# Optimization experiments

Hardware: AMD Instinct MI355X
Metric: run time of the kernel (lower is better)

The kernel has to match this reference:

```python
import jax, jax.numpy as jnp
import numpy as np

N_EXPERTS = 8
TOP_K = 2
D_MODEL = 1024
N_TOKENS = 8192


def setup_inputs() -> dict:
    key = jax.random.key(0)
    k1, k2, k3, k4, k5 = jax.random.split(key, 5)
    x = jax.random.normal(k1, (N_TOKENS, D_MODEL), dtype=jnp.float32)
    # router Linear(num_experts): weight [d, E], bias [E]
    Wr = jax.random.normal(k2, (D_MODEL, N_EXPERTS), dtype=jnp.float32) / np.sqrt(D_MODEL)
    br = jnp.zeros((N_EXPERTS,), dtype=jnp.float32)
    # per-expert Linear(d_model): stacked weights [E, d, d], biases [E, d]
    W = jax.random.normal(k3, (N_EXPERTS, D_MODEL, D_MODEL), dtype=jnp.float32) / np.sqrt(D_MODEL)
    b = jnp.zeros((N_EXPERTS, D_MODEL), dtype=jnp.float32)
    return {"x": x, "Wr": Wr, "br": br, "W": W, "b": b}


def reference(x, Wr, br, W, b):
    # --- route ---
    logits = x @ Wr + br                                  # [N, E]
    top_k_vals, top_k_idxs = jax.lax.top_k(logits, TOP_K)  # [N, k]
    top_k_gates = jax.nn.softmax(top_k_vals, axis=-1)      # [N, k]
    # --- experts (dense form of gather-dispatch; same math as routed compute) ---
    y_all = jnp.einsum('nd,edh->neh', x, W) + b            # [N, E, d]
    # --- gather routed expert outputs per slot ---
    y_k = jnp.take_along_axis(y_all, top_k_idxs[:, :, None], axis=1)  # [N, k, d]
    # --- weighted scatter-combine (reduce) ---
    out = jnp.sum(top_k_gates[:, :, None] * y_k, axis=1)   # [N, d]
    return out
```

## Files before the change

### kernel.cpp

```cpp
#include <hip/hip_runtime.h>
#include <hip/hip_bf16.h>


#define NTOK 8192
#define DM   1024
#define NEXP 8
#define CAP  8192
#define MAXT 136

typedef __attribute__((ext_vector_type(8))) short bf16x8;
typedef __attribute__((ext_vector_type(4))) float f32x4;

__device__ __forceinline__ unsigned short f2bf(float f) {
  unsigned u = __float_as_uint(f);
  unsigned r = (u + 0x7fffu + ((u >> 16) & 1u)) >> 16;
  return (unsigned short)r;
}
__device__ __forceinline__ float bf2f(unsigned short s) {
  return __uint_as_float(((unsigned)s) << 16);
}

__device__ __forceinline__ void gl_lds16(const void* g, void* l) {
  __builtin_amdgcn_global_load_lds(
      (const __attribute__((address_space(1))) unsigned int*)g,
      (__attribute__((address_space(3))) unsigned int*)l, 16, 0, 0);
}

__global__ __launch_bounds__(256) void transpose_w_kernel(
    const float* __restrict__ W, unsigned short* __restrict__ Wt) {
  __shared__ float tile[64][65];
  const int e = blockIdx.z;
  const int d0 = blockIdx.y * 64, h0 = blockIdx.x * 64;
  const float* Ws = W + (size_t)e * DM * DM;
  unsigned short* Wd = Wt + (size_t)e * DM * DM;
  const int r = threadIdx.x >> 4;
  const int c4 = (threadIdx.x & 15) * 4;
#pragma unroll
  for (int k = 0; k < 4; k++) {
    int row = r + k * 16;
    float4 v = *(const float4*)(Ws + (size_t)(d0 + row) * DM + h0 + c4);
    tile[row][c4 + 0] = v.x; tile[row][c4 + 1] = v.y;
    tile[row][c4 + 2] = v.z; tile[row][c4 + 3] = v.w;
  }
  __syncthreads();
#pragma unroll
  for (int k = 0; k < 4; k++) {
    int hrow = r + k * 16;
    ushort4 o;
    o.x = f2bf(tile[c4 + 0][hrow]);
    o.y = f2bf(tile[c4 + 1][hrow]);
    o.z = f2bf(tile[c4 + 2][hrow]);
    o.w = f2bf(tile[c4 + 3][hrow]);
    *(ushort4*)(Wd + (size_t)(h0 + hrow) * DM + d0 + c4) = o;
  }
}

__global__ __launch_bounds__(256) void router_compute_kernel(
    const float* __restrict__ x, const float* __restrict__ Wr,
    const float* __restrict__ br, unsigned short* __restrict__ xbf,
    int4* __restrict__ topk) {
  const int tid = threadIdx.x;
  const int wave = tid >> 6, lane = tid & 63;
  const int t = blockIdx.x * 4 + wave;
  const int c0 = lane * 16;
  const float* xr = x + (size_t)t * DM + c0;

  float v[16];
#pragma unroll
  for (int i = 0; i < 4; i++) {
    float4 f = *(const float4*)(xr + i * 4);
    v[i * 4 + 0] = f.x; v[i * 4 + 1] = f.y; v[i * 4 + 2] = f.z; v[i * 4 + 3] = f.w;
  }
  union { unsigned short s[8]; uint4 q; } pk;
#pragma unroll
  for (int half = 0; half < 2; half++) {
#pragma unroll
    for (int i = 0; i < 8; i++) pk.s[i] = f2bf(v[half * 8 + i]);
    *(uint4*)(xbf + (size_t)t * DM + c0 + half * 8) = pk.q;
  }
  float p[8] = {0, 0, 0, 0, 0, 0, 0, 0};
  const float* wr = Wr + (size_t)c0 * NEXP;
#pragma unroll
  for (int i = 0; i < 16; i++) {
    float xv = v[i];
    float4 wl = *(const float4*)(wr + i * 8);
    float4 wh = *(const float4*)(wr + i * 8 + 4);
    p[0] += xv * wl.x; p[1] += xv * wl.y; p[2] += xv * wl.z; p[3] += xv * wl.w;
    p[4] += xv * wh.x; p[5] += xv * wh.y; p[6] += xv * wh.z; p[7] += xv * wh.w;
  }
#pragma unroll
  for (int off = 32; off >= 1; off >>= 1) {
#pragma unroll
    for (int e = 0; e < 8; e++) p[e] += __shfl_xor(p[e], off, 64);
  }
  if (lane == 0) {
    float lg[8];
#pragma unroll
    for (int e = 0; e < 8; e++) lg[e] = p[e] + br[e];
    float v0 = lg[0]; int i0 = 0;
#pragma unroll
    for (int e = 1; e < 8; e++) if (lg[e] > v0) { v0 = lg[e]; i0 = e; }
    float v1 = -3.4e38f; int i1 = 0;
#pragma unroll
    for (int e = 0; e < 8; e++)
      if (e != i0 && lg[e] > v1) { v1 = lg[e]; i1 = e; }
    float ee = __expf(v1 - v0);
    float g0 = 1.0f / (1.0f + ee);
    float g1 = ee / (1.0f + ee);
    int4 rec;
    rec.x = i0; rec.y = i1;
    rec.z = __float_as_int(g0); rec.w = __float_as_int(g1);
    topk[t] = rec;
  }
}

__global__ __launch_bounds__(512) void scatter_kernel(
    const int4* __restrict__ topk, int* __restrict__ counts,
    int* __restrict__ tok, int2* __restrict__ pos) {
  __shared__ int lcnt[NEXP], lbase[NEXP];
  const int tid = threadIdx.x;
  if (tid < NEXP) lcnt[tid] = 0;
  __syncthreads();
  const int t = blockIdx.x * 512 + tid;
  int4 r = topk[t];
  int s0 = atomicAdd(&lcnt[r.x], 1);
  int s1 = atomicAdd(&lcnt[r.y], 1);
  __syncthreads();
  if (tid < NEXP) lbase[tid] = atomicAdd(&counts[tid], lcnt[tid]);
  __syncthreads();
  int p0 = lbase[r.x] + s0;
  int p1 = lbase[r.y] + s1;
  tok[r.x * CAP + p0] = t;
  tok[r.y * CAP + p1] = t;
  int2 pr; pr.x = p0; pr.y = p1;
  pos[t] = pr;
}

__global__ __launch_bounds__(64) void build_tiles_kernel(
    const int* __restrict__ counts, int* __restrict__ desc,
    int* __restrict__ ntiles, int* __restrict__ offset) {
  if (threadIdx.x == 0) {
    int idx = 0, off = 0;
#pragma unroll
    for (int e = 0; e < NEXP; e++) {
      offset[e] = off;
      off += counts[e];
      int nm = (counts[e] + 127) >> 7;
      for (int i = 0; i < nm; i++) desc[idx++] = (e << 16) | i;
    }
    *ntiles = idx;
  }
}

__global__ __launch_bounds__(256) void moe_gemm_kernel(
    const unsigned short* __restrict__ xbf, const unsigned short* __restrict__ wt,
    const int* __restrict__ counts, const int* __restrict__ offset,
    const int* __restrict__ tok, const int* __restrict__ desc,
    const int* __restrict__ ntiles, unsigned short* __restrict__ ybuf) {
  const int slot = blockIdx.y;
  if (slot >= *ntiles) return;
  const int dsc = desc[slot];
  const int e = dsc >> 16;
  const int m0 = (dsc & 0xffff) * 128;
  const int cnt = counts[e];
  const int n0 = blockIdx.x * 128;

  __shared__ __align__(16) unsigned short sA0[128 * 32];
  __shared__ __align__(16) unsigned short sB0[128 * 32];
  __shared__ __align__(16) unsigned short sA1[128 * 32];
  __shared__ __align__(16) unsigned short sB1[128 * 32];
  __shared__ int sTok[128];

  const int tid = threadIdx.x, wave = tid >> 6, lane = tid & 63;

  if (tid < 128) {
    int sr = m0 + tid;
    int cl = (sr < cnt) ? sr : (cnt - 1);
    sTok[tid] = tok[e * CAP + cl];
  }
  __syncthreads();

  const int rA1 = wave * 16 + (lane >> 2);
  const int rA2 = rA1 + 64;
  const int cch = lane & 3;
  const int cg1 = (cch ^ ((rA1 >> 1) & 3)) * 8;
  const int cg2 = (cch ^ ((rA2 >> 1) & 3)) * 8;
  const unsigned short* pA1 = xbf + (size_t)sTok[rA1] * DM + cg1;
  const unsigned short* pA2 = xbf + (size_t)sTok[rA2] * DM + cg2;
  const unsigned short* wte = wt + (size_t)e * DM * DM;
  const unsigned short* pB1 = wte + (size_t)(n0 + rA1) * DM + cg1;
  const unsigned short* pB2 = wte + (size_t)(n0 + rA2) * DM + cg2;
  const int lo1 = wave * 512, lo2 = (wave + 4) * 512;

  const int q = lane >> 4, ml = lane & 15;
  const int wm = (wave >> 1) * 64, wn = (wave & 1) * 64;
  int offA[4], offB[4];
#pragma unroll
  for (int i = 0; i < 4; i++) {
    int row = wm + i * 16 + ml;
    offA[i] = row * 32 + (q ^ ((row >> 1) & 3)) * 8;
    int rowb = wn + i * 16 + ml;
    offB[i] = rowb * 32 + (q ^ ((rowb >> 1) & 3)) * 8;
  }

  f32x4 acc[4][4] = {};

  for (int k0 = 0; k0 < DM; k0 += 64) {
    gl_lds16(pA1 + k0, sA0 + lo1);
    gl_lds16(pA2 + k0, sA0 + lo2);
    gl_lds16(pB1 + k0, sB0 + lo1);
    gl_lds16(pB2 + k0, sB0 + lo2);
    gl_lds16(pA1 + k0 + 32, sA1 + lo1);
    gl_lds16(pA2 + k0 + 32, sA1 + lo2);
    gl_lds16(pB1 + k0 + 32, sB1 + lo1);
    gl_lds16(pB2 + k0 + 32, sB1 + lo2);
    __syncthreads();
    bf16x8 af0[4], bf0[4], af1[4], bf1[4];
#pragma unroll
    for (int i = 0; i < 4; i++) {
      af0[i] = *(const bf16x8*)(sA0 + offA[i]);
      bf0[i] = *(const bf16x8*)(sB0 + offB[i]);
      af1[i] = *(const bf16x8*)(sA1 + offA[i]);
      bf1[i] = *(const bf16x8*)(sB1 + offB[i]);
    }
#pragma unroll
    for (int mt = 0; mt < 4; mt++)
#pragma unroll
      for (int nt = 0; nt < 4; nt++)
        acc[mt][nt] = __builtin_amdgcn_mfma_f32_16x16x32_bf16(
            af0[mt], bf0[nt], acc[mt][nt], 0, 0, 0);
#pragma unroll
    for (int mt = 0; mt < 4; mt++)
#pragma unroll
      for (int nt = 0; nt < 4; nt++)
        acc[mt][nt] = __builtin_amdgcn_mfma_f32_16x16x32_bf16(
            af1[mt], bf1[nt], acc[mt][nt], 0, 0, 0);
    __syncthreads();
  }

  const int yb = offset[e] + m0;
#pragma unroll
  for (int mt = 0; mt < 4; mt++) {
    int rbase = wm + mt * 16 + q * 4;
#pragma unroll
    for (int r = 0; r < 4; r++) {
      int row = rbase + r;
      if (m0 + row >= cnt) continue;
      unsigned short* yrow = ybuf + (size_t)(yb + row) * DM + n0;
#pragma unroll
      for (int nt = 0; nt < 4; nt++) {
        yrow[wn + nt * 16 + ml] = f2bf(acc[mt][nt][r]);
      }
    }
  }
}

__global__ __launch_bounds__(256) void combine_kernel(
    const unsigned short* __restrict__ ybuf, const int4* __restrict__ topk,
    const int2* __restrict__ pos, const int* __restrict__ offset,
    const float* __restrict__ bias, float* __restrict__ out) {
  const int t = blockIdx.x;
  const int c = threadIdx.x * 4;
  int4 r = topk[t];
  int2 p = pos[t];
  float g0 = __int_as_float(r.z), g1 = __int_as_float(r.w);
  int s0 = offset[r.x] + p.x;
  int s1 = offset[r.y] + p.y;
  ushort4 ya = *(const ushort4*)(ybuf + (size_t)s0 * DM + c);
  ushort4 yb = *(const ushort4*)(ybuf + (size_t)s1 * DM + c);
  float4 b0 = *(const float4*)(bias + (size_t)r.x * DM + c);
  float4 b1 = *(const float4*)(bias + (size_t)r.y * DM + c);
  float4 o;
  o.x = g0 * (bf2f(ya.x) + b0.x) + g1 * (bf2f(yb.x) + b1.x);
  o.y = g0 * (bf2f(ya.y) + b0.y) + g1 * (bf2f(yb.y) + b1.y);
  o.z = g0 * (bf2f(ya.z) + b0.z) + g1 * (bf2f(yb.z) + b1.z);
  o.w = g0 * (bf2f(ya.w) + b0.w) + g1 * (bf2f(yb.w) + b1.w);
  *(float4*)(out + (size_t)t * DM + c) = o;
}

extern "C" void kernel_launch(void* const* d_in, const int* in_sizes, int n_in,
                              void* d_out, int out_size, void* d_ws, size_t ws_size,
                              hipStream_t stream) {
  const float* x  = (const float*)d_in[0];
  const float* Wr = (const float*)d_in[1];
  const float* br = (const float*)d_in[2];
  const float* W  = (const float*)d_in[3];
  const float* b  = (const float*)d_in[4];
  float* out = (float*)d_out;

  char* ws = (char*)d_ws;
  unsigned short* xbf  = (unsigned short*)ws;
  unsigned short* wt   = (unsigned short*)(ws + (16u << 20));
  unsigned short* ybuf = (unsigned short*)(ws + (32u << 20));
  char* ctrl = ws + (64u << 20);
  int*   counts = (int*)ctrl;
  int*   ntiles = (int*)(ctrl + 64);
  int*   offset = (int*)(ctrl + 128);
  int*   desc   = (int*)(ctrl + 256);
  int*   tok    = (int*)(ctrl + 4096);
  int2*  pos    = (int2*)(ctrl + 4096 + (256u << 10));
  int4*  topk   = (int4*)(ctrl + 4096 + (320u << 10));

  hipMemsetAsync(counts, 0, 128, stream);

  transpose_w_kernel<<<dim3(16, 16, 8), 256, 0, stream>>>(W, wt);
  router_compute_kernel<<<NTOK / 4, 256, 0, stream>>>(x, Wr, br, xbf, topk);
  scatter_kernel<<<16, 512, 0, stream>>>(topk, counts, tok, pos);
  build_tiles_kernel<<<1, 64, 0, stream>>>(counts, desc, ntiles, offset);
  moe_gemm_kernel<<<dim3(8, MAXT), 256, 0, stream>>>(
      xbf, wt, counts, offset, tok, desc, ntiles, ybuf);
  combine_kernel<<<NTOK, 256, 0, stream>>>(ybuf, topk, pos, offset, b, out);
}
```

Measured before the change: 214.0 us.

## Widen weight-transpose tiles, swap GEMM grid order, drop shared token staging

The weight transpose now converts to bf16 before writing to LDS and uses 64x256 tiles, so each row of the output is written as a longer contiguous run. The MoE GEMM grid is reordered so consecutive blocks walk over M tiles for the same N column, which changes the order in which L2 sees weight and activation traffic. The shared-memory token index array and its barrier are removed, and each thread loads its two token indices directly. The smaller LDS stride of 260 shorts may cause bank conflicts on the scattered element writes.

```diff
diff --git a/kernel.cpp b/kernel.cpp
--- a/kernel.cpp
+++ b/kernel.cpp
@@ -28,30 +28,31 @@
 
 __global__ __launch_bounds__(256) void transpose_w_kernel(
     const float* __restrict__ W, unsigned short* __restrict__ Wt) {
-  __shared__ float tile[64][65];
+  __shared__ unsigned short L[64 * 260];
   const int e = blockIdx.z;
-  const int d0 = blockIdx.y * 64, h0 = blockIdx.x * 64;
+  const int d0 = blockIdx.y * 256, h0 = blockIdx.x * 64;
   const float* Ws = W + (size_t)e * DM * DM;
   unsigned short* Wd = Wt + (size_t)e * DM * DM;
-  const int r = threadIdx.x >> 4;
-  const int c4 = (threadIdx.x & 15) * 4;
-#pragma unroll
-  for (int k = 0; k < 4; k++) {
-    int row = r + k * 16;
-    float4 v = *(const float4*)(Ws + (size_t)(d0 + row) * DM + h0 + c4);
-    tile[row][c4 + 0] = v.x; tile[row][c4 + 1] = v.y;
-    tile[row][c4 + 2] = v.z; tile[row][c4 + 3] = v.w;
+  const int tid = threadIdx.x;
+  const int hh = (tid & 15) * 4;
+  const int dr = tid >> 4;
+#pragma unroll
+  for (int it = 0; it < 16; it++) {
+    int dd = it * 16 + dr;
+    float4 v = *(const float4*)(Ws + (size_t)(d0 + dd) * DM + h0 + hh);
+    L[(hh + 0) * 260 + dd] = f2bf(v.x);
+    L[(hh + 1) * 260 + dd] = f2bf(v.y);
+    L[(hh + 2) * 260 + dd] = f2bf(v.z);
+    L[(hh + 3) * 260 + dd] = f2bf(v.w);
   }
   __syncthreads();
-#pragma unroll
-  for (int k = 0; k < 4; k++) {
-    int hrow = r + k * 16;
-    ushort4 o;
-    o.x = f2bf(tile[c4 + 0][hrow]);
-    o.y = f2bf(tile[c4 + 1][hrow]);
-    o.z = f2bf(tile[c4 + 2][hrow]);
-    o.w = f2bf(tile[c4 + 3][hrow]);
-    *(ushort4*)(Wd + (size_t)(h0 + hrow) * DM + d0 + c4) = o;
+  const int dc = (tid & 63) * 4;
+  const int hw = tid >> 6;
+#pragma unroll
+  for (int it = 0; it < 16; it++) {
+    int hr = it * 4 + hw;
+    ushort4 o = *(const ushort4*)(&L[hr * 260 + dc]);
+    *(ushort4*)(Wd + (size_t)(h0 + hr) * DM + d0 + dc) = o;
   }
 }
 
@@ -157,36 +158,32 @@
     const int* __restrict__ counts, const int* __restrict__ offset,
     const int* __restrict__ tok, const int* __restrict__ desc,
     const int* __restrict__ ntiles, unsigned short* __restrict__ ybuf) {
-  const int slot = blockIdx.y;
+  const int slot = blockIdx.x;
   if (slot >= *ntiles) return;
   const int dsc = desc[slot];
   const int e = dsc >> 16;
   const int m0 = (dsc & 0xffff) * 128;
   const int cnt = counts[e];
-  const int n0 = blockIdx.x * 128;
+  const int n0 = blockIdx.y * 128;
 
   __shared__ __align__(16) unsigned short sA0[128 * 32];
   __shared__ __align__(16) unsigned short sB0[128 * 32];
   __shared__ __align__(16) unsigned short sA1[128 * 32];
   __shared__ __align__(16) unsigned short sB1[128 * 32];
-  __shared__ int sTok[128];
 
   const int tid = threadIdx.x, wave = tid >> 6, lane = tid & 63;
-
-  if (tid < 128) {
-    int sr = m0 + tid;
-    int cl = (sr < cnt) ? sr : (cnt - 1);
-    sTok[tid] = tok[e * CAP + cl];
-  }
-  __syncthreads();
 
   const int rA1 = wave * 16 + (lane >> 2);
   const int rA2 = rA1 + 64;
   const int cch = lane & 3;
   const int cg1 = (cch ^ ((rA1 >> 1) & 3)) * 8;
   const int cg2 = (cch ^ ((rA2 >> 1) & 3)) * 8;
-  const unsigned short* pA1 = xbf + (size_t)sTok[rA1] * DM + cg1;
-  const unsigned short* pA2 = xbf + (size_t)sTok[rA2] * DM + cg2;
+  int r1 = m0 + rA1; if (r1 >= cnt) r1 = cnt - 1;
+  int r2 = m0 + rA2; if (r2 >= cnt) r2 = cnt - 1;
+  const int t1 = tok[e * CAP + r1];
+  const int t2 = tok[e * CAP + r2];
+  const unsigned short* pA1 = xbf + (size_t)t1 * DM + cg1;
+  const unsigned short* pA2 = xbf + (size_t)t2 * DM + cg2;
   const unsigned short* wte = wt + (size_t)e * DM * DM;
   const unsigned short* pB1 = wte + (size_t)(n0 + rA1) * DM + cg1;
   const unsigned short* pB2 = wte + (size_t)(n0 + rA2) * DM + cg2;
@@ -303,11 +300,11 @@
 
   hipMemsetAsync(counts, 0, 128, stream);
 
-  transpose_w_kernel<<<dim3(16, 16, 8), 256, 0, stream>>>(W, wt);
+  transpose_w_kernel<<<dim3(16, 4, 8), 256, 0, stream>>>(W, wt);
   router_compute_kernel<<<NTOK / 4, 256, 0, stream>>>(x, Wr, br, xbf, topk);
   scatter_kernel<<<16, 512, 0, stream>>>(topk, counts, tok, pos);
   build_tiles_kernel<<<1, 64, 0, stream>>>(counts, desc, ntiles, offset);
-  moe_gemm_kernel<<<dim3(8, MAXT), 256, 0, stream>>>(
+  moe_gemm_kernel<<<dim3(MAXT, 8), 256, 0, stream>>>(
       xbf, wt, counts, offset, tok, desc, ntiles, ybuf);
   combine_kernel<<<NTOK, 256, 0, stream>>>(ybuf, topk, pos, offset, b, out);
 }
```

New measurement: 215.1 us. About the same (+0.5%).
